# Optimization experiments

Hardware: AMD Instinct MI355X
Metric: run time of the kernel (lower is better)

Reference implementation:

```python
import jax, jax.numpy as jnp
import numpy as np

EMBED_DIM = 1024
NHEAD = 16
HEAD_DIM = EMBED_DIM // NHEAD
BASE = 10000.0


def rope_tables(seq_len, dim):
    # dim = head_dim; freqs over dim/2
    inv_freq = 1.0 / (BASE ** (jnp.arange(0, dim, 2, dtype=jnp.float32) / dim))
    t = jnp.arange(seq_len, dtype=jnp.float32)
    freqs = jnp.einsum('i,j->ij', t, inv_freq)          # [S, dim/2]
    return jnp.cos(freqs), jnp.sin(freqs)


def apply_rope(x, cos, sin):
    # x: [B,H,S,D]; cos/sin: [S, D/2] broadcast over B,H
    x1, x2 = jnp.split(x, 2, axis=-1)
    return jnp.concatenate((x1 * cos - x2 * sin, x1 * sin + x2 * cos), axis=-1)


def setup_inputs() -> dict:
    key = jax.random.key(0)
    ks = jax.random.split(key, 7)
    B, S, E = 2, 2048, EMBED_DIM
    scale = 1.0 / np.sqrt(E)
    return {
        'query': jax.random.normal(ks[0], (B, S, E), dtype=jnp.float32),
        'key':   jax.random.normal(ks[1], (B, S, E), dtype=jnp.float32),
        'value': jax.random.normal(ks[2], (B, S, E), dtype=jnp.float32),
        'Wq': jax.random.normal(ks[3], (E, E), dtype=jnp.float32) * scale,
        'Wk': jax.random.normal(ks[4], (E, E), dtype=jnp.float32) * scale,
        'Wv': jax.random.normal(ks[5], (E, E), dtype=jnp.float32) * scale,
        'Wo': jax.random.normal(ks[6], (E, E), dtype=jnp.float32) * scale,
    }


def reference(query, key, value, Wq, Wk, Wv, Wo):
    B, Sq, E = query.shape
    Skv = key.shape[1]
    H, D = NHEAD, HEAD_DIM
    # projections (nn.Linear: x @ W.T), split heads -> [B,H,S,D]
    q = (query @ Wq.T).reshape(B, Sq, H, D).transpose(0, 2, 1, 3)
    k = (key   @ Wk.T).reshape(B, Skv, H, D).transpose(0, 2, 1, 3)
    v = (value @ Wv.T).reshape(B, Skv, H, D).transpose(0, 2, 1, 3)
    cos, sin = rope_tables(Sq, D)
    q = apply_rope(q, cos, sin)
    k = apply_rope(k, cos, sin)
    scores = jnp.einsum('bhqd,bhkd->bhqk', q, k) / jnp.sqrt(jnp.asarray(D, q.dtype))
    probs = jax.nn.softmax(scores, axis=-1)
    out = jnp.einsum('bhqk,bhkd->bhqd', probs, v)
    out = out.transpose(0, 2, 1, 3).reshape(B, Sq, E)
    return out @ Wo.T
```

## Files before the change

### kernel.cpp

```cpp
#include <hip/hip_runtime.h>

typedef __bf16 bf16_t;
typedef __attribute__((ext_vector_type(8))) __bf16 bf16x8;
typedef __attribute__((ext_vector_type(4))) __bf16 bf16x4;
typedef __attribute__((ext_vector_type(4))) float f32x4;
typedef __attribute__((ext_vector_type(16))) float f32x16;
typedef __attribute__((ext_vector_type(4))) int i32x4;

#define GAS __attribute__((address_space(1)))
#define LAS __attribute__((address_space(3)))

__device__ __forceinline__ void gload_lds16(const bf16_t* g, bf16_t* l) {
  __builtin_amdgcn_global_load_lds((const GAS char*)(const char*)g,
                                   (LAS char*)(char*)l, 16, 0, 0);
}

__global__ __launch_bounds__(256) void f2bf_w(const float* __restrict__ wq,
                                              const float* __restrict__ wk,
                                              const float* __restrict__ wv,
                                              const float* __restrict__ wo,
                                              bf16_t* __restrict__ wsb,
                                              float* __restrict__ ct,
                                              float* __restrict__ st) {
  if (blockIdx.x >= 4096) {
    const int gid = (blockIdx.x - 4096) * 256 + threadIdx.x;
    const int s = gid >> 5, j = gid & 31;
    const float inv = exp2f(-(float)j * (13.287712379549449f / 32.0f));
    const float ang = (float)s * inv;
    ct[gid] = cosf(ang);
    st[gid] = sinf(ang);
    return;
  }
  const size_t W = 1048576;
  const size_t gid = (size_t)(blockIdx.x * 256 + threadIdx.x) * 4;
  const float* src; size_t off;
  if      (gid < W)     { src = wq; off = gid; }
  else if (gid < 2 * W) { src = wk; off = gid - W; }
  else if (gid < 3 * W) { src = wv; off = gid - 2 * W; }
  else                  { src = wo; off = gid - 3 * W; }
  const float4 vv = *(const float4*)(src + off);
  bf16x4 o;
  o[0] = (bf16_t)vv.x; o[1] = (bf16_t)vv.y; o[2] = (bf16_t)vv.z; o[3] = (bf16_t)vv.w;
  *(bf16x4*)(wsb + gid) = o;
}

template <int EPI, int AF32>
__device__ __forceinline__ void gemm_bt_body(const void* __restrict__ Ap,
                                             const bf16_t* __restrict__ Bm,
                                             void* __restrict__ Cout,
                                             const float* __restrict__ ctab,
                                             const float* __restrict__ stab,
                                             const float scale,
                                             const int m0, const int n0,
                                             bf16_t* __restrict__ sm) {
  constexpr int K = 1024, N = 1024;
  bf16_t* As = sm;
  bf16_t* Bs = sm + 8192;
  const int tid = threadIdx.x;
  const int lane = tid & 63;
  const int w = tid >> 6;
  const int wr = w >> 1, wc = w & 1;
  const int g = lane >> 4, c = lane & 15;
  const bf16_t* Ab = (const bf16_t*)Ap;
  const float* Af = (const float*)Ap;

  f32x4 acc[4][4] = {};

  float4 areg[8];
  if (AF32) {
#pragma unroll
    for (int i = 0; i < 4; ++i) {
      const int idx8 = i * 256 + tid;
      const int row = idx8 >> 3, j8 = idx8 & 7;
      const size_t base = (size_t)(m0 + row) * K + j8 * 8;
      areg[2 * i]     = *(const float4*)(Af + base);
      areg[2 * i + 1] = *(const float4*)(Af + base + 4);
    }
  }

  for (int k0 = 0; k0 < K; k0 += 64) {
    if (AF32) {
#pragma unroll
      for (int i = 0; i < 4; ++i) {
        const int idx8 = i * 256 + tid;
        const int row = idx8 >> 3, j8 = idx8 & 7;
        bf16x8 o;
        o[0] = (bf16_t)areg[2 * i].x;     o[1] = (bf16_t)areg[2 * i].y;
        o[2] = (bf16_t)areg[2 * i].z;     o[3] = (bf16_t)areg[2 * i].w;
        o[4] = (bf16_t)areg[2 * i + 1].x; o[5] = (bf16_t)areg[2 * i + 1].y;
        o[6] = (bf16_t)areg[2 * i + 1].z; o[7] = (bf16_t)areg[2 * i + 1].w;
        *(bf16x8*)(As + row * 64 + ((j8 ^ (row & 7)) * 8)) = o;
      }
#pragma unroll
      for (int i = 0; i < 4; ++i) {
        const int chunk0 = (i * 4 + w) * 64;
        const int idx = chunk0 + lane;
        const int row = idx >> 3;
        const int sw = (idx & 7) ^ (row & 7);
        gload_lds16(Bm + (size_t)(n0 + row) * K + (k0 + sw * 8), Bs + chunk0 * 8);
      }
    } else {
#pragma unroll
      for (int i = 0; i < 4; ++i) {
        const int chunk0 = (i * 4 + w) * 64;
        const int idx = chunk0 + lane;
        const int row = idx >> 3;
        const int sw = (idx & 7) ^ (row & 7);
        gload_lds16(Ab + (size_t)(m0 + row) * K + (k0 + sw * 8), As + chunk0 * 8);
        gload_lds16(Bm + (size_t)(n0 + row) * K + (k0 + sw * 8), Bs + chunk0 * 8);
      }
    }
    __syncthreads();
    if (AF32 && k0 + 64 < K) {
#pragma unroll
      for (int i = 0; i < 4; ++i) {
        const int idx8 = i * 256 + tid;
        const int row = idx8 >> 3, j8 = idx8 & 7;
        const size_t base = (size_t)(m0 + row) * K + (k0 + 64) + j8 * 8;
        areg[2 * i]     = *(const float4*)(Af + base);
        areg[2 * i + 1] = *(const float4*)(Af + base + 4);
      }
    }
    bf16x8 af[4][2], bfr[4][2];
#pragma unroll
    for (int t = 0; t < 4; ++t) {
#pragma unroll
      for (int kc = 0; kc < 2; ++kc) {
        const int ra = wr * 64 + t * 16 + c;
        af[t][kc] = *(const bf16x8*)(As + ra * 64 + (((kc * 4 + g) ^ (ra & 7)) * 8));
        const int rb = wc * 64 + t * 16 + c;
        bfr[t][kc] = *(const bf16x8*)(Bs + rb * 64 + (((kc * 4 + g) ^ (rb & 7)) * 8));
      }
    }
#pragma unroll
    for (int mi = 0; mi < 4; ++mi)
#pragma unroll
      for (int ni = 0; ni < 4; ++ni)
#pragma unroll
        for (int kc = 0; kc < 2; ++kc)
          acc[mi][ni] = __builtin_amdgcn_mfma_f32_16x16x32_bf16(
              af[mi][kc], bfr[ni][kc], acc[mi][ni], 0, 0, 0);
    __syncthreads();
  }
  if (EPI == 2) {
#pragma unroll
    for (int mi = 0; mi < 4; ++mi)
#pragma unroll
      for (int ni = 0; ni < 4; ++ni)
#pragma unroll
        for (int r = 0; r < 4; ++r) {
          const int lr = wr * 64 + mi * 16 + g * 4 + r;
          const int lc = wc * 64 + ni * 16 + c;
          sm[lc * 136 + lr] = (bf16_t)acc[mi][ni][r];
        }
    __syncthreads();
    bf16_t* Vt = (bf16_t*)Cout;
    const int bb = m0 >> 11, sbase = m0 & 2047;
#pragma unroll
    for (int it = 0; it < 8; ++it) {
      const int idx = it * 256 + tid;
      const int lc = idx >> 4, kk = idx & 15;
      const bf16x8 vv = *(const bf16x8*)(sm + lc * 136 + kk * 8);
      *(bf16x8*)(Vt + ((size_t)(bb * 1024 + n0 + lc)) * 2048 + sbase + kk * 8) = vv;
    }
    return;
  }
  if (EPI == 0 && ctab != nullptr) {
    bf16_t* Cb = (bf16_t*)Cout;
#pragma unroll
    for (int mi = 0; mi < 4; ++mi)
#pragma unroll
      for (int r = 0; r < 4; ++r) {
        const int grow = m0 + wr * 64 + mi * 16 + g * 4 + r;
        const int s = grow & 2047;
        const float* crow = ctab + s * 32;
        const float* srow = stab + s * 32;
#pragma unroll
        for (int ni = 0; ni < 2; ++ni) {
          const int j = ni * 16 + c;
          const float cc = crow[j], ss = srow[j];
          const float x1 = acc[mi][ni][r];
          const float x2 = acc[mi][ni + 2][r];
          const int gcol = n0 + wc * 64 + j;
          Cb[(size_t)grow * N + gcol]      = (bf16_t)((x1 * cc - x2 * ss) * scale);
          Cb[(size_t)grow * N + gcol + 32] = (bf16_t)((x1 * ss + x2 * cc) * scale);
        }
      }
    return;
  }
#pragma unroll
  for (int mi = 0; mi < 4; ++mi)
#pragma unroll
    for (int ni = 0; ni < 4; ++ni)
#pragma unroll
      for (int r = 0; r < 4; ++r) {
        const int grow = m0 + wr * 64 + mi * 16 + g * 4 + r;
        const int gcol = n0 + wc * 64 + ni * 16 + c;
        const float v = acc[mi][ni][r];
        if (EPI == 0) ((bf16_t*)Cout)[(size_t)grow * N + gcol] = (bf16_t)v;
        else          ((float*)Cout)[(size_t)grow * N + gcol] = v;
      }
}

__global__ __launch_bounds__(256) void qkv_gemm(
    const float* __restrict__ qf, const float* __restrict__ kf, const float* __restrict__ vf,
    const bf16_t* __restrict__ wqb, const bf16_t* __restrict__ wkb, const bf16_t* __restrict__ wvb,
    bf16_t* __restrict__ Qp, bf16_t* __restrict__ Kp, bf16_t* __restrict__ Vtp,
    const float* __restrict__ ctab, const float* __restrict__ stab) {
  __shared__ __align__(16) bf16_t sm[17408];
  const int bid = blockIdx.x;
  const int wg = (bid & 7) * 96 + (bid >> 3);
  const int z = wg >> 8;
  const int rem = wg & 255;
  const int m0 = (rem >> 3) * 128;
  const int n0 = (rem & 7) * 128;
  if (z == 0) {
    gemm_bt_body<0, 1>(qf, wqb, Qp, ctab, stab, 0.18033688011112042f, m0, n0, sm);
  } else if (z == 1) {
    gemm_bt_body<0, 1>(kf, wkb, Kp, ctab, stab, 1.0f, m0, n0, sm);
  } else {
    gemm_bt_body<2, 1>(vf, wvb, Vtp, nullptr, nullptr, 1.0f, m0, n0, sm);
  }
}

__global__ __launch_bounds__(256) void out_gemm(const bf16_t* __restrict__ A,
                                                const bf16_t* __restrict__ B,
                                                float* __restrict__ C) {
  __shared__ __align__(16) bf16_t sm[17408];
  const int bid = blockIdx.x;
  const int wg = (bid & 7) * 32 + (bid >> 3);
  const int m0 = (wg >> 3) * 128;
  const int n0 = (wg & 7) * 128;
  gemm_bt_body<1, 0>(A, B, C, nullptr, nullptr, 1.0f, m0, n0, sm);
}

__global__ __launch_bounds__(512, 4) void flash_attn(const bf16_t* __restrict__ Q,
                                                     const bf16_t* __restrict__ Kr,
                                                     const bf16_t* __restrict__ Vt,
                                                     bf16_t* __restrict__ O) {
  __shared__ __align__(16) bf16_t Ksm[2][2][64 * 64];
  __shared__ __align__(16) bf16_t Vsm[2][2][64 * 64];
  const int tid = threadIdx.x, lane = tid & 63, w = tid >> 6;
  const int wl = w & 3, g = w >> 2;
  const int li = lane & 31, hi = lane >> 5;
  const int bid = blockIdx.x;
  const int xcd = bid & 7, slot = bid >> 3;
  const int bh = xcd * 4 + (slot >> 4);
  const int qb = slot & 15;
  const int b = bh >> 4, h = bh & 15;
  const int q0 = qb * 128 + wl * 32;

  bf16x8 qf[4];
  {
    const size_t qaddr = ((size_t)b * 2048 + q0 + li) * 1024 + h * 64 + hi * 8;
#pragma unroll
    for (int ks = 0; ks < 4; ++ks) qf[ks] = *(const bf16x8*)(Q + qaddr + ks * 16);
  }

  bf16x8 ones;
#pragma unroll
  for (int j = 0; j < 8; ++j) ones[j] = (bf16_t)1.0f;

  const f32x16 zero16 = {};
  f32x16 o0 = zero16, o1 = zero16, osum = zero16;

  const size_t kbase  = (size_t)b * 2048 * 1024 + h * 64;
  const size_t vtbase = (size_t)((b * 16 + h) * 64) * 2048;
  const int kv_off = g * 1024;

#define STAGE(buf, kv0)                                                          \
  {                                                                              \
    _Pragma("unroll")                                                            \
    for (int i = 0; i < 2; ++i) {                                                \
      const int chunk0 = (i * 4 + wl) * 64;                                      \
      const int idx = chunk0 + lane;                                             \
      const int row = idx >> 3;                                                  \
      const int sw = ((idx & 7) ^ (row & 7)) * 8;                                \
      gload_lds16(Kr + kbase + (size_t)((kv0) + row) * 1024 + sw,                \
                  &Ksm[g][buf][chunk0 * 8]);                                     \
      gload_lds16(Vt + vtbase + (size_t)row * 2048 + (kv0) + sw,                 \
                  &Vsm[g][buf][chunk0 * 8]);                                     \
    }                                                                            \
  }

#define CVTPK(dst, lo_, hi_) \
  asm("v_cvt_pk_bf16_f32 %0, %1, %2" : "=v"(dst) : "v"(lo_), "v"(hi_))
#define PLSWAP(x_, y_) \
  asm volatile("v_permlane32_swap_b32 %0, %1" : "+v"(x_), "+v"(y_))

  STAGE(0, kv_off)
  asm volatile("s_waitcnt vmcnt(0)" ::: "memory");
  __builtin_amdgcn_s_barrier();
  int cur = 0;
  for (int t = 0; t < 16; ++t) {
    if (t < 15) STAGE(cur ^ 1, kv_off + (t + 1) * 64)

    f32x16 p0 = zero16, p1 = zero16;
    __builtin_amdgcn_s_setprio(1);
#pragma unroll
    for (int ks = 0; ks < 4; ++ks) {
      const int r0 = li;
      const bf16x8 kf0 = *(const bf16x8*)(&Ksm[g][cur][r0 * 64 + (((ks * 2 + hi) ^ (r0 & 7)) * 8)]);
      p0 = __builtin_amdgcn_mfma_f32_32x32x16_bf16(kf0, qf[ks], p0, 0, 0, 0);
      const int r1 = 32 + li;
      const bf16x8 kf1 = *(const bf16x8*)(&Ksm[g][cur][r1 * 64 + (((ks * 2 + hi) ^ (r1 & 7)) * 8)]);
      p1 = __builtin_amdgcn_mfma_f32_32x32x16_bf16(kf1, qf[ks], p1, 0, 0, 0);
    }
    __builtin_amdgcn_s_setprio(0);

#pragma unroll
    for (int j = 0; j < 16; ++j) { p0[j] = exp2f(p0[j]); p1[j] = exp2f(p1[j]); }

    bf16x8 pa[4];
#pragma unroll
    for (int ks = 0; ks < 4; ++ks) {
      int A_, B_, C_, D_;
      if (ks == 0) { CVTPK(A_, p0[0], p0[1]); CVTPK(B_, p0[2], p0[3]);
                     CVTPK(C_, p0[4], p0[5]); CVTPK(D_, p0[6], p0[7]); }
      else if (ks == 1) { CVTPK(A_, p0[8],  p0[9]);  CVTPK(B_, p0[10], p0[11]);
                          CVTPK(C_, p0[12], p0[13]); CVTPK(D_, p0[14], p0[15]); }
      else if (ks == 2) { CVTPK(A_, p1[0], p1[1]); CVTPK(B_, p1[2], p1[3]);
                          CVTPK(C_, p1[4], p1[5]); CVTPK(D_, p1[6], p1[7]); }
      else { CVTPK(A_, p1[8],  p1[9]);  CVTPK(B_, p1[10], p1[11]);
             CVTPK(C_, p1[12], p1[13]); CVTPK(D_, p1[14], p1[15]); }
      PLSWAP(A_, C_);
      PLSWAP(B_, D_);
      i32x4 iv; iv[0] = A_; iv[1] = B_; iv[2] = C_; iv[3] = D_;
      pa[ks] = __builtin_bit_cast(bf16x8, iv);
    }

    __builtin_amdgcn_s_setprio(1);
#pragma unroll
    for (int ks = 0; ks < 4; ++ks) {
      const int r0 = li;
      const bf16x8 vf0 = *(const bf16x8*)(&Vsm[g][cur][r0 * 64 + (((ks * 2 + hi) ^ (r0 & 7)) * 8)]);
      o0 = __builtin_amdgcn_mfma_f32_32x32x16_bf16(pa[ks], vf0, o0, 0, 0, 0);
      const int r1 = 32 + li;
      const bf16x8 vf1 = *(const bf16x8*)(&Vsm[g][cur][r1 * 64 + (((ks * 2 + hi) ^ (r1 & 7)) * 8)]);
      o1 = __builtin_amdgcn_mfma_f32_32x32x16_bf16(pa[ks], vf1, o1, 0, 0, 0);
      osum = __builtin_amdgcn_mfma_f32_32x32x16_bf16(pa[ks], ones, osum, 0, 0, 0);
    }
    __builtin_amdgcn_s_setprio(0);

    if (t < 15) {
      asm volatile("s_waitcnt vmcnt(0)" ::: "memory");
      __builtin_amdgcn_s_barrier();
    }
    cur ^= 1;
  }
#undef STAGE
#undef CVTPK
#undef PLSWAP

  float* Osm = (float*)&Ksm[0][0][0];
  float* lsm = (float*)&Vsm[0][0][0];

  if (g == 1) {
    float* Ow = Osm + wl * 2048;
#pragma unroll
    for (int reg = 0; reg < 16; ++reg) {
      const int ql = (reg & 3) + 8 * (reg >> 2) + 4 * hi;
      Ow[ql * 64 + li]      = o0[reg];
      Ow[ql * 64 + 32 + li] = o1[reg];
      if (li == 0) lsm[wl * 32 + ql] = osum[reg];
    }
  }
  __syncthreads();
  if (g == 0) {
    const float* Ow = Osm + wl * 2048;
#pragma unroll
    for (int reg = 0; reg < 16; ++reg) {
      const int ql = (reg & 3) + 8 * (reg >> 2) + 4 * hi;
      const float rl = 1.0f / (osum[reg] + lsm[wl * 32 + ql]);
      const size_t base = ((size_t)b * 2048 + q0 + ql) * 1024 + h * 64 + li;
      O[base]      = (bf16_t)((o0[reg] + Ow[ql * 64 + li])      * rl);
      O[base + 32] = (bf16_t)((o1[reg] + Ow[ql * 64 + 32 + li]) * rl);
    }
  }
}

extern "C" void kernel_launch(void* const* d_in, const int* in_sizes, int n_in,
                              void* d_out, int out_size, void* d_ws, size_t ws_size,
                              hipStream_t stream) {
  (void)in_sizes; (void)n_in; (void)out_size; (void)ws_size;
  const float* q_in = (const float*)d_in[0];
  const float* k_in = (const float*)d_in[1];
  const float* v_in = (const float*)d_in[2];
  const float* wq = (const float*)d_in[3];
  const float* wk = (const float*)d_in[4];
  const float* wv = (const float*)d_in[5];
  const float* wo = (const float*)d_in[6];
  float* out = (float*)d_out;

  bf16_t* ws = (bf16_t*)d_ws;
  const size_t T = 4096ull * 1024ull;
  const size_t W = 1024ull * 1024ull;
  bf16_t* wqb = ws;
  bf16_t* wkb = wqb + W;
  bf16_t* wvb = wkb + W;
  bf16_t* wob = wvb + W;
  bf16_t* Qp  = wob + W;
  bf16_t* Kp  = Qp + T;
  bf16_t* Vtp = Kp + T;
  bf16_t* AO  = Vtp + T;
  float* ctab = (float*)(AO + T);
  float* stab = ctab + 65536;

  f2bf_w<<<4352, 256, 0, stream>>>(wq, wk, wv, wo, wqb, ctab, stab);
  qkv_gemm<<<768, 256, 0, stream>>>(q_in, k_in, v_in, wqb, wkb, wvb, Qp, Kp, Vtp,
                                    ctab, stab);
  flash_attn<<<512, 512, 0, stream>>>(Qp, Kp, Vtp, AO);
  out_gemm<<<256, 256, 0, stream>>>(AO, wob, out);
}
```

Baseline: 129.9 us.

## Software-pipeline QKV GEMM with double-buffered B tiles and two-deep A prefetch

Restructures the fp32-A QKV projection GEMM main loop into a fully unrolled 16-step pipeline. B tiles are double-buffered in LDS via async global-to-LDS loads, and fp32 A tiles are prefetched two iterations ahead in registers, with explicit vmcnt/lgkmcnt waits and raw barriers replacing __syncthreads. The goal is to hide global load latency behind MFMA work. In exchange it uses more LDS (24576 bf16) and more registers, which may lower occupancy, and it relies on hand-tuned waitcnt counts being correct.

Result: no change. 129.9 us (-0.0%).

```diff
diff --git a/kernel.cpp b/kernel.cpp
--- a/kernel.cpp
+++ b/kernel.cpp
@@ -9,6 +9,8 @@
 
 #define GAS __attribute__((address_space(1)))
 #define LAS __attribute__((address_space(3)))
+
+#define CFENCE() asm volatile("" ::: "memory")
 
 __device__ __forceinline__ void gload_lds16(const bf16_t* g, bf16_t* l) {
   __builtin_amdgcn_global_load_lds((const GAS char*)(const char*)g,
@@ -55,7 +57,7 @@
                                              bf16_t* __restrict__ sm) {
   constexpr int K = 1024, N = 1024;
   bf16_t* As = sm;
-  bf16_t* Bs = sm + 8192;
+  bf16_t* Bs0 = sm + 8192;
   const int tid = threadIdx.x;
   const int lane = tid & 63;
   const int w = tid >> 6;
@@ -66,40 +68,103 @@
 
   f32x4 acc[4][4] = {};
 
-  float4 areg[8];
   if (AF32) {
+    float4 aregs[2][8];
+#pragma unroll
+    for (int i = 0; i < 4; ++i) {
+      const int chunk0 = (i * 4 + w) * 64;
+      const int idx = chunk0 + lane;
+      const int row = idx >> 3;
+      const int sw = (idx & 7) ^ (row & 7);
+      gload_lds16(Bm + (size_t)(n0 + row) * K + sw * 8, Bs0 + chunk0 * 8);
+    }
+    CFENCE();
 #pragma unroll
     for (int i = 0; i < 4; ++i) {
       const int idx8 = i * 256 + tid;
       const int row = idx8 >> 3, j8 = idx8 & 7;
       const size_t base = (size_t)(m0 + row) * K + j8 * 8;
-      areg[2 * i]     = *(const float4*)(Af + base);
-      areg[2 * i + 1] = *(const float4*)(Af + base + 4);
-    }
-  }
-
-  for (int k0 = 0; k0 < K; k0 += 64) {
-    if (AF32) {
+      aregs[0][2 * i]     = *(const float4*)(Af + base);
+      aregs[0][2 * i + 1] = *(const float4*)(Af + base + 4);
+    }
+    CFENCE();
+#pragma unroll
+    for (int i = 0; i < 4; ++i) {
+      const int idx8 = i * 256 + tid;
+      const int row = idx8 >> 3, j8 = idx8 & 7;
+      const size_t base = (size_t)(m0 + row) * K + 64 + j8 * 8;
+      aregs[1][2 * i]     = *(const float4*)(Af + base);
+      aregs[1][2 * i + 1] = *(const float4*)(Af + base + 4);
+    }
+    asm volatile("s_waitcnt vmcnt(8)" ::: "memory");
+
+#pragma unroll
+    for (int t = 0; t < 16; ++t) {
+      const int pc = t & 1;
+      bf16_t* BsC = Bs0 + pc * 8192;
+      bf16_t* BsN = Bs0 + (pc ^ 1) * 8192;
+      if (t > 0) { __builtin_amdgcn_s_barrier(); CFENCE(); }
 #pragma unroll
       for (int i = 0; i < 4; ++i) {
         const int idx8 = i * 256 + tid;
         const int row = idx8 >> 3, j8 = idx8 & 7;
         bf16x8 o;
-        o[0] = (bf16_t)areg[2 * i].x;     o[1] = (bf16_t)areg[2 * i].y;
-        o[2] = (bf16_t)areg[2 * i].z;     o[3] = (bf16_t)areg[2 * i].w;
-        o[4] = (bf16_t)areg[2 * i + 1].x; o[5] = (bf16_t)areg[2 * i + 1].y;
-        o[6] = (bf16_t)areg[2 * i + 1].z; o[7] = (bf16_t)areg[2 * i + 1].w;
+        o[0] = (bf16_t)aregs[pc][2 * i].x;     o[1] = (bf16_t)aregs[pc][2 * i].y;
+        o[2] = (bf16_t)aregs[pc][2 * i].z;     o[3] = (bf16_t)aregs[pc][2 * i].w;
+        o[4] = (bf16_t)aregs[pc][2 * i + 1].x; o[5] = (bf16_t)aregs[pc][2 * i + 1].y;
+        o[6] = (bf16_t)aregs[pc][2 * i + 1].z; o[7] = (bf16_t)aregs[pc][2 * i + 1].w;
         *(bf16x8*)(As + row * 64 + ((j8 ^ (row & 7)) * 8)) = o;
       }
-#pragma unroll
-      for (int i = 0; i < 4; ++i) {
-        const int chunk0 = (i * 4 + w) * 64;
-        const int idx = chunk0 + lane;
-        const int row = idx >> 3;
-        const int sw = (idx & 7) ^ (row & 7);
-        gload_lds16(Bm + (size_t)(n0 + row) * K + (k0 + sw * 8), Bs + chunk0 * 8);
-      }
-    } else {
+      CFENCE();
+      if (t < 15) {
+#pragma unroll
+        for (int i = 0; i < 4; ++i) {
+          const int chunk0 = (i * 4 + w) * 64;
+          const int idx = chunk0 + lane;
+          const int row = idx >> 3;
+          const int sw = (idx & 7) ^ (row & 7);
+          gload_lds16(Bm + (size_t)(n0 + row) * K + ((t + 1) * 64 + sw * 8),
+                      BsN + chunk0 * 8);
+        }
+      }
+      CFENCE();
+      if (t < 14) {
+#pragma unroll
+        for (int i = 0; i < 4; ++i) {
+          const int idx8 = i * 256 + tid;
+          const int row = idx8 >> 3, j8 = idx8 & 7;
+          const size_t base = (size_t)(m0 + row) * K + (t + 2) * 64 + j8 * 8;
+          aregs[pc][2 * i]     = *(const float4*)(Af + base);
+          aregs[pc][2 * i + 1] = *(const float4*)(Af + base + 4);
+        }
+      }
+      asm volatile("s_waitcnt lgkmcnt(0)" ::: "memory");
+      __builtin_amdgcn_s_barrier();
+      CFENCE();
+      bf16x8 af[4][2], bfr[4][2];
+#pragma unroll
+      for (int tt = 0; tt < 4; ++tt)
+#pragma unroll
+        for (int kc = 0; kc < 2; ++kc) {
+          const int ra = wr * 64 + tt * 16 + c;
+          af[tt][kc] = *(const bf16x8*)(As + ra * 64 + (((kc * 4 + g) ^ (ra & 7)) * 8));
+          const int rb = wc * 64 + tt * 16 + c;
+          bfr[tt][kc] = *(const bf16x8*)(BsC + rb * 64 + (((kc * 4 + g) ^ (rb & 7)) * 8));
+        }
+#pragma unroll
+      for (int mi = 0; mi < 4; ++mi)
+#pragma unroll
+        for (int ni = 0; ni < 4; ++ni)
+#pragma unroll
+          for (int kc = 0; kc < 2; ++kc)
+            acc[mi][ni] = __builtin_amdgcn_mfma_f32_16x16x32_bf16(
+                af[mi][kc], bfr[ni][kc], acc[mi][ni], 0, 0, 0);
+      if (t < 14)       asm volatile("s_waitcnt vmcnt(8)" ::: "memory");
+      else if (t == 14) asm volatile("s_waitcnt vmcnt(0)" ::: "memory");
+    }
+    __syncthreads();
+  } else {
+    for (int k0 = 0; k0 < K; k0 += 64) {
 #pragma unroll
       for (int i = 0; i < 4; ++i) {
         const int chunk0 = (i * 4 + w) * 64;
@@ -107,41 +172,31 @@
         const int row = idx >> 3;
         const int sw = (idx & 7) ^ (row & 7);
         gload_lds16(Ab + (size_t)(m0 + row) * K + (k0 + sw * 8), As + chunk0 * 8);
-        gload_lds16(Bm + (size_t)(n0 + row) * K + (k0 + sw * 8), Bs + chunk0 * 8);
-      }
-    }
-    __syncthreads();
-    if (AF32 && k0 + 64 < K) {
-#pragma unroll
-      for (int i = 0; i < 4; ++i) {
-        const int idx8 = i * 256 + tid;
-        const int row = idx8 >> 3, j8 = idx8 & 7;
-        const size_t base = (size_t)(m0 + row) * K + (k0 + 64) + j8 * 8;
-        areg[2 * i]     = *(const float4*)(Af + base);
-        areg[2 * i + 1] = *(const float4*)(Af + base + 4);
-      }
-    }
-    bf16x8 af[4][2], bfr[4][2];
-#pragma unroll
-    for (int t = 0; t < 4; ++t) {
-#pragma unroll
-      for (int kc = 0; kc < 2; ++kc) {
-        const int ra = wr * 64 + t * 16 + c;
-        af[t][kc] = *(const bf16x8*)(As + ra * 64 + (((kc * 4 + g) ^ (ra & 7)) * 8));
-        const int rb = wc * 64 + t * 16 + c;
-        bfr[t][kc] = *(const bf16x8*)(Bs + rb * 64 + (((kc * 4 + g) ^ (rb & 7)) * 8));
-      }
-    }
-#pragma unroll
-    for (int mi = 0; mi < 4; ++mi)
-#pragma unroll
-      for (int ni = 0; ni < 4; ++ni)
-#pragma unroll
-        for (int kc = 0; kc < 2; ++kc)
-          acc[mi][ni] = __builtin_amdgcn_mfma_f32_16x16x32_bf16(
-              af[mi][kc], bfr[ni][kc], acc[mi][ni], 0, 0, 0);
-    __syncthreads();
-  }
+        gload_lds16(Bm + (size_t)(n0 + row) * K + (k0 + sw * 8), Bs0 + chunk0 * 8);
+      }
+      __syncthreads();
+      bf16x8 af[4][2], bfr[4][2];
+#pragma unroll
+      for (int tt = 0; tt < 4; ++tt)
+#pragma unroll
+        for (int kc = 0; kc < 2; ++kc) {
+          const int ra = wr * 64 + tt * 16 + c;
+          af[tt][kc] = *(const bf16x8*)(As + ra * 64 + (((kc * 4 + g) ^ (ra & 7)) * 8));
+          const int rb = wc * 64 + tt * 16 + c;
+          bfr[tt][kc] = *(const bf16x8*)(Bs0 + rb * 64 + (((kc * 4 + g) ^ (rb & 7)) * 8));
+        }
+#pragma unroll
+      for (int mi = 0; mi < 4; ++mi)
+#pragma unroll
+        for (int ni = 0; ni < 4; ++ni)
+#pragma unroll
+          for (int kc = 0; kc < 2; ++kc)
+            acc[mi][ni] = __builtin_amdgcn_mfma_f32_16x16x32_bf16(
+                af[mi][kc], bfr[ni][kc], acc[mi][ni], 0, 0, 0);
+      __syncthreads();
+    }
+  }
+
   if (EPI == 2) {
 #pragma unroll
     for (int mi = 0; mi < 4; ++mi)
@@ -207,7 +262,7 @@
     const bf16_t* __restrict__ wqb, const bf16_t* __restrict__ wkb, const bf16_t* __restrict__ wvb,
     bf16_t* __restrict__ Qp, bf16_t* __restrict__ Kp, bf16_t* __restrict__ Vtp,
     const float* __restrict__ ctab, const float* __restrict__ stab) {
-  __shared__ __align__(16) bf16_t sm[17408];
+  __shared__ __align__(16) bf16_t sm[24576];
   const int bid = blockIdx.x;
   const int wg = (bid & 7) * 96 + (bid >> 3);
   const int z = wg >> 8;
```
